# Performance work log

Hardware: AMD Instinct MI355X
Metric: run time of the kernel (lower is better)

Reference implementation:

```python
import jax, jax.numpy as jnp
import numpy as np

SPINS = (16, 16)
D_FEAT = 1024
H1 = (4096, 4096, 2048)
H2 = (2048, 1)


def _pair_idx(n):
    # Matches: idx_h1 = [i for i in range(n-1) for j in range(n-1-i)]
    #          h2 = concat(h[k:] for k in 1..n-1)  -> all ordered pairs (i, j), i < j
    i = np.repeat(np.arange(n - 1), np.arange(n - 1, 0, -1))
    j = np.concatenate([np.arange(k + 1, n) for k in range(n - 1)])
    return i.astype(np.int32), j.astype(np.int32)


def setup_inputs():
    key = jax.random.key(0)
    ks = jax.random.split(key, 6)

    def w(k, fi, fo, scale):
        return (scale / np.sqrt(fi)).astype(np.float32) * jax.random.normal(k, (fi, fo), jnp.float32)

    d_in = 2 * D_FEAT
    return {
        "h_one": jax.random.normal(ks[0], (sum(SPINS), D_FEAT), jnp.float32),
        "w1_0": w(ks[1], d_in, H1[0], np.float32(np.sqrt(2.0))),
        "b1_0": jnp.zeros((H1[0],), jnp.float32),
        "w1_1": w(ks[2], H1[0], H1[1], np.float32(np.sqrt(2.0))),
        "b1_1": jnp.zeros((H1[1],), jnp.float32),
        # final mlp1 layer scaled so |hidden| ~ 2: keeps the pair-product finite in fp32
        "w1_2": w(ks[3], H1[1], H1[2], np.float32(2.0)),
        "b1_2": jnp.zeros((H1[2],), jnp.float32),
        "w2_0": w(ks[4], H1[2], H2[0], np.float32(1.0)),
        "b2_0": jnp.zeros((H2[0],), jnp.float32),
        "w2_1": w(ks[5], H2[0], H2[1], np.float32(1.0)),
        "b2_1": jnp.zeros((H2[1],), jnp.float32),
    }


def reference(h_one, w1_0, b1_0, w1_1, b1_1, w1_2, b1_2, w2_0, b2_0, w2_1, b2_1):
    def mlp1(x):  # silu hidden layers, linear output
        x = jax.nn.silu(x @ w1_0 + b1_0)
        x = jax.nn.silu(x @ w1_1 + b1_1)
        return x @ w1_2 + b1_2

    def mlp2(x):  # tanh hidden layer, linear scalar output
        x = jnp.tanh(x @ w2_0 + b2_0)
        return x @ w2_1 + b2_1

    sumlogA = jnp.float32(0.0)
    off = 0
    for n in SPINS:  # fixed, small, structurally distinct loop over spin channels
        h = h_one[off:off + n]
        off += n
        ii, jj = _pair_idx(n)  # static numpy indices
        h1, h2 = h[ii], h[jj]  # [P, D] pairwise gathers, P = n*(n-1)/2
        hidden = mlp1(jnp.concatenate([h1, h2], axis=-1)) \
               - mlp1(jnp.concatenate([h2, h1], axis=-1))  # antisymmetric in (h1, h2)
        a = jnp.prod(hidden, axis=0)  # product-reduce over pairs -> [H1[-1]]
        A = mlp2(a)                   # [1]
        sumlogA = sumlogA + jnp.log(jnp.abs(A)).squeeze()
    return sumlogA
```

## Files before the change

### kernel.cpp

```cpp
#include <hip/hip_runtime.h>
#include <hip/hip_bf16.h>
#include <math.h>


typedef __attribute__((ext_vector_type(8))) short short8;
typedef __attribute__((ext_vector_type(4))) float floatx4;

#define AS1 __attribute__((address_space(1)))
#define AS3 __attribute__((address_space(3)))
#define GLD16(g, l) __builtin_amdgcn_global_load_lds((AS1 const unsigned int*)(g), (AS3 unsigned int*)(l), 16, 0, 0)

__device__ __forceinline__ float silu_f(float x) {
    return x / (1.0f + __expf(-x));
}

__device__ __forceinline__ void split2(float x, unsigned short& hi, unsigned short& lo) {
    unsigned u = __float_as_uint(x);
    unsigned r = u + 0x7FFFu + ((u >> 16) & 1u);
    unsigned short h = (unsigned short)(r >> 16);
    float hf = __uint_as_float((unsigned)h << 16);
    float rem = x - hf;
    unsigned u2 = __float_as_uint(rem);
    unsigned r2 = u2 + 0x7FFFu + ((u2 >> 16) & 1u);
    hi = h;
    lo = (unsigned short)(r2 >> 16);
}

__global__ __launch_bounds__(256)
void transpose_split_all(const float* __restrict__ w10, const float* __restrict__ w11,
                         const float* __restrict__ w12, const float* __restrict__ h_one,
                         unsigned short* __restrict__ t10h, unsigned short* __restrict__ t10l,
                         unsigned short* __restrict__ t11h, unsigned short* __restrict__ t11l,
                         unsigned short* __restrict__ t12h, unsigned short* __restrict__ t12l,
                         unsigned short* __restrict__ Ah, unsigned short* __restrict__ Al) {
    const int t = threadIdx.x;
    int id = blockIdx.x;

    if (id >= 8192) {
        const int base = (id - 8192) * 4096 + t * 16;
        #pragma unroll
        for (int j = 0; j < 4; ++j) {
            const int f = base + 4 * j;
            const int r = f >> 10;
            const int c = f & 1023;
            floatx4 v = __builtin_nontemporal_load((const floatx4*)&h_one[f]);
            ushort4 hv, lv;
            split2(v.x, hv.x, lv.x);
            split2(v.y, hv.y, lv.y);
            split2(v.z, hv.z, lv.z);
            split2(v.w, hv.w, lv.w);
            const size_t o1 = (size_t)r * 2048 + c;
            const size_t o2 = (size_t)(64 + r) * 2048 + 1024 + c;
            *(ushort4*)&Ah[o1] = hv;
            *(ushort4*)&Al[o1] = lv;
            *(ushort4*)&Ah[o2] = hv;
            *(ushort4*)&Al[o2] = lv;
        }
        return;
    }

    const float* W;
    unsigned short *Th, *Tl;
    int K, N, nt, kt;
    if (id < 2048)       { W = w10; Th = t10h; Tl = t10l; K = 2048; N = 4096; nt = id & 63; kt = id >> 6; }
    else if (id < 6144)  { id -= 2048; W = w11; Th = t11h; Tl = t11l; K = 4096; N = 4096; nt = id & 63; kt = id >> 6; }
    else                 { id -= 6144; W = w12; Th = t12h; Tl = t12l; K = 4096; N = 2048; nt = id & 31; kt = id >> 5; }

    __shared__ float tile[64][65];
    const int n0 = nt * 64;
    const int k0 = kt * 64;

    const int lrow = t >> 4;
    const int lcol = (t & 15) * 4;
    #pragma unroll
    for (int p = 0; p < 4; ++p) {
        const int r = p * 16 + lrow;
        floatx4 v = __builtin_nontemporal_load((const floatx4*)&W[(size_t)(k0 + r) * N + n0 + lcol]);
        tile[r][lcol + 0] = v.x;
        tile[r][lcol + 1] = v.y;
        tile[r][lcol + 2] = v.z;
        tile[r][lcol + 3] = v.w;
    }
    __syncthreads();

    const int srow0 = t >> 3;
    const int koff  = (t & 7) * 8;
    #pragma unroll
    for (int p = 0; p < 2; ++p) {
        const int sn = p * 32 + srow0;
        unsigned short hv[8], lv[8];
        #pragma unroll
        for (int kk = 0; kk < 8; ++kk)
            split2(tile[koff + kk][sn], hv[kk], lv[kk]);
        unsigned short* dh = &Th[(size_t)(n0 + sn) * K + k0 + koff];
        unsigned short* dl = &Tl[(size_t)(n0 + sn) * K + k0 + koff];
        *(short8*)dh = *(short8*)&hv[0];
        *(short8*)dl = *(short8*)&lv[0];
    }
}

__global__ __launch_bounds__(256, 2)
void gemm128(const unsigned short* __restrict__ Ah, const unsigned short* __restrict__ Al,
             const unsigned short* __restrict__ Bh, const unsigned short* __restrict__ Bl,
             int K, float* __restrict__ Cpart, int N, int Mtot, int kc)
{
    __shared__ __align__(16) unsigned short As[2][128][32];
    __shared__ __align__(16) unsigned short Bs[2][128][32];

    const int tid  = threadIdx.x;
    const int lane = tid & 63;
    const int wid  = tid >> 6;
    const int n0 = blockIdx.x * 128;
    const int m0 = blockIdx.y * 128;
    const int kbase = blockIdx.z * kc;

    const int srow   = wid * 32 + (lane >> 2);
    const int schunk = (lane & 3) ^ ((srow >> 1) & 3);
    const unsigned short* gA0h = Ah + (size_t)(m0 + srow) * K + kbase + schunk * 8;
    const unsigned short* gA1h = gA0h + (size_t)16 * K;
    const unsigned short* gA0l = Al + (size_t)(m0 + srow) * K + kbase + schunk * 8;
    const unsigned short* gA1l = gA0l + (size_t)16 * K;
    const unsigned short* gB0h = Bh + (size_t)(n0 + srow) * K + kbase + schunk * 8;
    const unsigned short* gB1h = gB0h + (size_t)16 * K;
    const unsigned short* gB0l = Bl + (size_t)(n0 + srow) * K + kbase + schunk * 8;
    const unsigned short* gB1l = gB0l + (size_t)16 * K;
    unsigned short* lA0h = &As[0][wid * 32][0];
    unsigned short* lA1h = &As[0][wid * 32 + 16][0];
    unsigned short* lA0l = &As[1][wid * 32][0];
    unsigned short* lA1l = &As[1][wid * 32 + 16][0];
    unsigned short* lB0h = &Bs[0][wid * 32][0];
    unsigned short* lB1h = &Bs[0][wid * 32 + 16][0];
    unsigned short* lB0l = &Bs[1][wid * 32][0];
    unsigned short* lB1l = &Bs[1][wid * 32 + 16][0];

    const int mhalf = wid >> 1;
    const int nhalf = wid & 1;
    const int lm = lane & 15;
    const int q  = lane >> 4;
    int aoffs[4], boffs[4];
    #pragma unroll
    for (int f = 0; f < 4; ++f) {
        int arow = mhalf * 64 + f * 16 + lm;
        int aslot = q ^ ((arow >> 1) & 3);
        aoffs[f] = arow * 32 + aslot * 8;
        int brow = nhalf * 64 + f * 16 + lm;
        int bslot = q ^ ((brow >> 1) & 3);
        boffs[f] = brow * 32 + bslot * 8;
    }
    const unsigned short* AsF = &As[0][0][0];
    const unsigned short* BsF = &Bs[0][0][0];

    floatx4 acc[4][4];
    #pragma unroll
    for (int ms = 0; ms < 4; ++ms)
        #pragma unroll
        for (int ns = 0; ns < 4; ++ns)
            acc[ms][ns] = (floatx4){0.f, 0.f, 0.f, 0.f};

    const int S = kc >> 5;
    for (int s = 0; s < S; ++s) {
        const int ko = s << 5;
        __syncthreads();
        GLD16(gA0h + ko, lA0h);
        GLD16(gA1h + ko, lA1h);
        GLD16(gA0l + ko, lA0l);
        GLD16(gA1l + ko, lA1l);
        GLD16(gB0h + ko, lB0h);
        GLD16(gB1h + ko, lB1h);
        GLD16(gB0l + ko, lB0l);
        GLD16(gB1l + ko, lB1l);
        __syncthreads();

        short8 afh[4], afl[4], bfh[4], bfl[4];
        #pragma unroll
        for (int f = 0; f < 4; ++f) {
            afh[f] = *(const short8*)(AsF + aoffs[f]);
            afl[f] = *(const short8*)(AsF + 4096 + aoffs[f]);
            bfh[f] = *(const short8*)(BsF + boffs[f]);
            bfl[f] = *(const short8*)(BsF + 4096 + boffs[f]);
        }
        #pragma unroll
        for (int ms = 0; ms < 4; ++ms)
            #pragma unroll
            for (int ns = 0; ns < 4; ++ns)
                acc[ms][ns] = __builtin_amdgcn_mfma_f32_16x16x32_bf16(afh[ms], bfh[ns], acc[ms][ns], 0, 0, 0);
        #pragma unroll
        for (int ms = 0; ms < 4; ++ms)
            #pragma unroll
            for (int ns = 0; ns < 4; ++ns)
                acc[ms][ns] = __builtin_amdgcn_mfma_f32_16x16x32_bf16(afl[ms], bfh[ns], acc[ms][ns], 0, 0, 0);
        #pragma unroll
        for (int ms = 0; ms < 4; ++ms)
            #pragma unroll
            for (int ns = 0; ns < 4; ++ns)
                acc[ms][ns] = __builtin_amdgcn_mfma_f32_16x16x32_bf16(afh[ms], bfl[ns], acc[ms][ns], 0, 0, 0);
    }

    float* Cp = Cpart + (size_t)blockIdx.z * Mtot * N;
    const int lr = (lane >> 4) * 4;
    #pragma unroll
    for (int ms = 0; ms < 4; ++ms)
        #pragma unroll
        for (int ns = 0; ns < 4; ++ns)
            #pragma unroll
            for (int r = 0; r < 4; ++r)
                Cp[(size_t)(m0 + mhalf * 64 + ms * 16 + lr + r) * N + n0 + nhalf * 64 + ns * 16 + lm] = acc[ms][ns][r];
}

__global__ __launch_bounds__(256)
void build_y1_kernel(const float* __restrict__ PQ, const float* __restrict__ b1,
                     unsigned short* __restrict__ Y1h, unsigned short* __restrict__ Y1l) {
    const int r = blockIdx.x;
    const int g = r / 240;
    const int rem = r % 240;
    const int o = rem / 120;
    const int p = rem % 120;
    int i = 0, pp = p, cnt = 15;
    while (pp >= cnt) { pp -= cnt; cnt--; i++; }
    const int j = i + 1 + pp;
    const int ai = g * 16 + (o ? j : i);
    const int bi = g * 16 + (o ? i : j);
    const size_t chunk4 = (size_t)128 * 4096 / 4;
    const float4* Pr0 = (const float4*)(PQ + (size_t)ai * 4096);
    const float4* Qr0 = (const float4*)(PQ + (size_t)(64 + bi) * 4096);
    const float4* Br  = (const float4*)b1;
    for (int c = threadIdx.x; c < 1024; c += 256) {
        float4 bv = Br[c];
        float s0 = bv.x, s1 = bv.y, s2 = bv.z, s3 = bv.w;
        #pragma unroll
        for (int cc = 0; cc < 4; ++cc) {
            float4 pv = Pr0[c + cc * chunk4];
            float4 qv = Qr0[c + cc * chunk4];
            s0 += pv.x + qv.x;
            s1 += pv.y + qv.y;
            s2 += pv.z + qv.z;
            s3 += pv.w + qv.w;
        }
        s0 = silu_f(s0);
        s1 = silu_f(s1);
        s2 = silu_f(s2);
        s3 = silu_f(s3);
        ushort4 hv, lv;
        split2(s0, hv.x, lv.x);
        split2(s1, hv.y, lv.y);
        split2(s2, hv.z, lv.z);
        split2(s3, hv.w, lv.w);
        *(ushort4*)&Y1h[(size_t)r * 4096 + c * 4] = hv;
        *(ushort4*)&Y1l[(size_t)r * 4096 + c * 4] = lv;
    }
}

__global__ __launch_bounds__(256)
void reduce4_silu_split(const float* __restrict__ Part, const float* __restrict__ bias,
                        unsigned short* __restrict__ Yh, unsigned short* __restrict__ Yl) {
    const size_t idx = (size_t)blockIdx.x * 256 + threadIdx.x;
    const size_t stride4 = (size_t)512 * 4096 / 4;
    const float4* p = (const float4*)Part;
    float4 v0 = p[idx], v1 = p[idx + stride4], v2 = p[idx + 2 * stride4], v3 = p[idx + 3 * stride4];
    const int col = (int)((idx * 4) & 4095);
    float4 b = *(const float4*)&bias[col];
    float s0 = silu_f(v0.x + v1.x + v2.x + v3.x + b.x);
    float s1 = silu_f(v0.y + v1.y + v2.y + v3.y + b.y);
    float s2 = silu_f(v0.z + v1.z + v2.z + v3.z + b.z);
    float s3 = silu_f(v0.w + v1.w + v2.w + v3.w + b.w);
    ushort4 hv, lv;
    split2(s0, hv.x, lv.x);
    split2(s1, hv.y, lv.y);
    split2(s2, hv.z, lv.z);
    split2(s3, hv.w, lv.w);
    *(ushort4*)&Yh[idx * 4] = hv;
    *(ushort4*)&Yl[idx * 4] = lv;
}

__global__ __launch_bounds__(256)
void reduce8_bias(const float* __restrict__ Part, const float* __restrict__ bias,
                  float* __restrict__ Hb) {
    const size_t idx = (size_t)blockIdx.x * 256 + threadIdx.x;
    const size_t stride4 = (size_t)512 * 2048 / 4;
    const float4* p = (const float4*)Part;
    float4 s = p[idx];
    #pragma unroll
    for (int c = 1; c < 8; ++c) {
        float4 v = p[idx + c * stride4];
        s.x += v.x; s.y += v.y; s.z += v.z; s.w += v.w;
    }
    const int col = (int)((idx * 4) & 2047);
    float4 b = *(const float4*)&bias[col];
    s.x += b.x; s.y += b.y; s.z += b.z; s.w += b.w;
    *(float4*)&Hb[idx * 4] = s;
}

__global__ __launch_bounds__(256)
void reduce_prod_kernel(const float* __restrict__ H, float* __restrict__ a_part) {
    const int g = blockIdx.y;
    const int cz = blockIdx.z;
    const int c = blockIdx.x * 256 + threadIdx.x;
    const float* base = H + (size_t)g * 240 * 2048 + c;
    float prod = 1.0f;
    const int p0 = cz * 30;
    for (int p = p0; p < p0 + 30; ++p) {
        float f = base[(size_t)p * 2048] - base[(size_t)(120 + p) * 2048];
        prod *= f;
    }
    a_part[(size_t)((g << 2) | cz) * 2048 + c] = prod;
}

__global__ __launch_bounds__(256)
void mlp2_acc2_kernel(const float* __restrict__ a_part, const float* __restrict__ W,
                      float* __restrict__ Part2) {
    __shared__ float a0s[128], a1s[128];
    const int kc = blockIdx.y, nc = blockIdx.x, t = threadIdx.x;
    if (t < 128) {
        const int k = kc * 128 + t;
        a0s[t] = a_part[k] * a_part[2048 + k] * a_part[4096 + k] * a_part[6144 + k];
        a1s[t] = a_part[8192 + k] * a_part[10240 + k] * a_part[12288 + k] * a_part[14336 + k];
    }
    __syncthreads();
    const int n = nc * 256 + t;
    const float* Wp = W + (size_t)(kc * 128) * 2048 + n;
    float s0 = 0.f, s1 = 0.f;
    #pragma unroll 8
    for (int kk = 0; kk < 128; ++kk) {
        float w = Wp[(size_t)kk * 2048];
        s0 = fmaf(a0s[kk], w, s0);
        s1 = fmaf(a1s[kk], w, s1);
    }
    Part2[kc * 4096 + n] = s0;
    Part2[kc * 4096 + 2048 + n] = s1;
}

__global__ __launch_bounds__(256)
void finalize_kernel(const float* __restrict__ Part2, const float* __restrict__ b2_0,
                     const float* __restrict__ w2_1, const float* __restrict__ b2_1,
                     float* __restrict__ out) {
    __shared__ float red[256];
    const int tid = threadIdx.x;
    float result = 0.0f;
    for (int g = 0; g < 2; ++g) {
        float s = 0.f;
        for (int n = tid; n < 2048; n += 256) {
            float acc = b2_0[n];
            #pragma unroll
            for (int kc = 0; kc < 16; ++kc)
                acc += Part2[kc * 4096 + g * 2048 + n];
            s += tanhf(acc) * w2_1[n];
        }
        red[tid] = s;
        __syncthreads();
        for (int off = 128; off > 0; off >>= 1) {
            if (tid < off) red[tid] += red[tid + off];
            __syncthreads();
        }
        if (tid == 0) result += logf(fabsf(red[0] + b2_1[0]));
        __syncthreads();
    }
    if (tid == 0) out[0] = result;
}

extern "C" void kernel_launch(void* const* d_in, const int* in_sizes, int n_in,
                              void* d_out, int out_size, void* d_ws, size_t ws_size,
                              hipStream_t stream) {
    const float* h_one = (const float*)d_in[0];
    const float* w1_0  = (const float*)d_in[1];
    const float* b1_0  = (const float*)d_in[2];
    const float* w1_1  = (const float*)d_in[3];
    const float* b1_1  = (const float*)d_in[4];
    const float* w1_2  = (const float*)d_in[5];
    const float* b1_2  = (const float*)d_in[6];
    const float* w2_0  = (const float*)d_in[7];
    const float* b2_0  = (const float*)d_in[8];
    const float* w2_1  = (const float*)d_in[9];
    const float* b2_1  = (const float*)d_in[10];
    float* out = (float*)d_out;

    char* ws = (char*)d_ws;
    unsigned short* W10t_h = (unsigned short*)ws;
    unsigned short* W10t_l = W10t_h + (size_t)4096 * 2048;
    float*          PartL1 = (float*)ws;
    ws += (size_t)4096 * 2048 * 2 * 2;
    unsigned short* W11t_h = (unsigned short*)ws;
    unsigned short* W11t_l = W11t_h + (size_t)4096 * 4096;
    float*          PartL2 = (float*)ws;
    ws += (size_t)4096 * 4096 * 2 * 2;
    unsigned short* W12t_h = (unsigned short*)ws;
    unsigned short* W12t_l = W12t_h + (size_t)2048 * 4096;
    ws += (size_t)2048 * 4096 * 2 * 2;
    unsigned short* Ah  = (unsigned short*)ws;  ws += (size_t)128 * 2048 * 2;
    unsigned short* Al  = (unsigned short*)ws;  ws += (size_t)128 * 2048 * 2;
    float* PQ  = (float*)ws;                    ws += (size_t)4 * 128 * 4096 * 4;
    unsigned short* Y1h = (unsigned short*)ws;  ws += (size_t)512 * 4096 * 2;
    unsigned short* Y1l = (unsigned short*)ws;  ws += (size_t)512 * 4096 * 2;
    unsigned short* Y2h = (unsigned short*)ws;  ws += (size_t)512 * 4096 * 2;
    unsigned short* Y2l = (unsigned short*)ws;  ws += (size_t)512 * 4096 * 2;
    float* Hb    = (float*)ws;                  ws += (size_t)512 * 2048 * 4;
    float* a_part = (float*)ws;                 ws += (size_t)8 * 2048 * 4;
    float* Part2 = (float*)ws;                  ws += (size_t)16 * 2 * 2048 * 4;

    hipMemsetAsync(Ah, 0, (size_t)128 * 2048 * 2 * 2, stream);
    transpose_split_all<<<8200, 256, 0, stream>>>(w1_0, w1_1, w1_2, h_one,
                                                  W10t_h, W10t_l, W11t_h, W11t_l,
                                                  W12t_h, W12t_l, Ah, Al);

    gemm128<<<dim3(32, 1, 4), 256, 0, stream>>>(Ah, Al, W10t_h, W10t_l, 2048,
                                                PQ, 4096, 128, 512);
    build_y1_kernel<<<480, 256, 0, stream>>>(PQ, b1_0, Y1h, Y1l);

    gemm128<<<dim3(32, 4, 4), 256, 0, stream>>>(Y1h, Y1l, W11t_h, W11t_l, 4096,
                                                PartL1, 4096, 512, 1024);
    reduce4_silu_split<<<2048, 256, 0, stream>>>(PartL1, b1_1, Y2h, Y2l);

    gemm128<<<dim3(16, 4, 8), 256, 0, stream>>>(Y2h, Y2l, W12t_h, W12t_l, 4096,
                                                PartL2, 2048, 512, 512);
    reduce8_bias<<<1024, 256, 0, stream>>>(PartL2, b1_2, Hb);

    reduce_prod_kernel<<<dim3(8, 2, 4), 256, 0, stream>>>(Hb, a_part);
    mlp2_acc2_kernel<<<dim3(8, 16), 256, 0, stream>>>(a_part, w2_0, Part2);
    finalize_kernel<<<1, 256, 0, stream>>>(Part2, b2_0, w2_1, b2_1, out);
}
```

Before: 332.4 us.

## Fuse split-K reductions into GEMM epilogues via last-block atomic counters

Removes the separate reduce4_silu_split, reduce8_bias and finalize kernels. Each split-K GEMM block now bumps a per-tile atomic counter, and the last block to finish a tile sums all partials, adds the bias, and applies SiLU plus the bf16 split or writes fp32. The mlp2 kernel uses the same last-block pattern to run the final tanh, dot product and log. This saves kernel launches and the extra full passes over partial buffers, at the cost of threadfences, atomics, and a serial tail in the last block of each tile.

```diff
diff --git a/kernel.cpp b/kernel.cpp
--- a/kernel.cpp
+++ b/kernel.cpp
@@ -102,7 +102,10 @@
 __global__ __launch_bounds__(256, 2)
 void gemm128(const unsigned short* __restrict__ Ah, const unsigned short* __restrict__ Al,
              const unsigned short* __restrict__ Bh, const unsigned short* __restrict__ Bl,
-             int K, float* __restrict__ Cpart, int N, int Mtot, int kc)
+             int K, float* __restrict__ Cpart, int N, int Mtot, int kc,
+             int mode, unsigned* __restrict__ cnt, const float* __restrict__ bias,
+             unsigned short* __restrict__ Yh, unsigned short* __restrict__ Yl,
+             float* __restrict__ Fout)
 {
     __shared__ __align__(16) unsigned short As[2][128][32];
     __shared__ __align__(16) unsigned short Bs[2][128][32];
@@ -205,6 +208,48 @@
             #pragma unroll
             for (int r = 0; r < 4; ++r)
                 Cp[(size_t)(m0 + mhalf * 64 + ms * 16 + lr + r) * N + n0 + nhalf * 64 + ns * 16 + lm] = acc[ms][ns][r];
+
+    if (mode == 0) return;
+
+    __threadfence();
+    __syncthreads();
+    __shared__ unsigned winflag;
+    if (tid == 0) {
+        const unsigned tileid = blockIdx.y * gridDim.x + blockIdx.x;
+        winflag = (atomicAdd(&cnt[tileid], 1u) == gridDim.z - 1u) ? 1u : 0u;
+    }
+    __syncthreads();
+    if (!winflag) return;
+    __threadfence();
+
+    const int zparts = (int)gridDim.z;
+    const size_t zs4 = ((size_t)Mtot * N) >> 2;
+    const float4* P4 = (const float4*)Cpart;
+    const float4* B4 = (const float4*)bias;
+    for (int e = tid; e < 128 * 32; e += 256) {
+        const int row = e >> 5;
+        const int c4  = e & 31;
+        const size_t fidx = (((size_t)(m0 + row) * N) >> 2) + (size_t)(n0 >> 2) + c4;
+        float4 s = P4[fidx];
+        for (int z = 1; z < zparts; ++z) {
+            float4 v = P4[fidx + (size_t)z * zs4];
+            s.x += v.x; s.y += v.y; s.z += v.z; s.w += v.w;
+        }
+        float4 b = B4[(n0 >> 2) + c4];
+        s.x += b.x; s.y += b.y; s.z += b.z; s.w += b.w;
+        if (mode == 1) {
+            ushort4 hv, lv;
+            split2(silu_f(s.x), hv.x, lv.x);
+            split2(silu_f(s.y), hv.y, lv.y);
+            split2(silu_f(s.z), hv.z, lv.z);
+            split2(silu_f(s.w), hv.w, lv.w);
+            const size_t o = (size_t)(m0 + row) * N + n0 + c4 * 4;
+            *(ushort4*)&Yh[o] = hv;
+            *(ushort4*)&Yl[o] = lv;
+        } else {
+            *(float4*)&Fout[(size_t)(m0 + row) * N + n0 + c4 * 4] = s;
+        }
+    }
 }
 
 __global__ __launch_bounds__(256)
@@ -251,46 +296,6 @@
 }
 
 __global__ __launch_bounds__(256)
-void reduce4_silu_split(const float* __restrict__ Part, const float* __restrict__ bias,
-                        unsigned short* __restrict__ Yh, unsigned short* __restrict__ Yl) {
-    const size_t idx = (size_t)blockIdx.x * 256 + threadIdx.x;
-    const size_t stride4 = (size_t)512 * 4096 / 4;
-    const float4* p = (const float4*)Part;
-    float4 v0 = p[idx], v1 = p[idx + stride4], v2 = p[idx + 2 * stride4], v3 = p[idx + 3 * stride4];
-    const int col = (int)((idx * 4) & 4095);
-    float4 b = *(const float4*)&bias[col];
-    float s0 = silu_f(v0.x + v1.x + v2.x + v3.x + b.x);
-    float s1 = silu_f(v0.y + v1.y + v2.y + v3.y + b.y);
-    float s2 = silu_f(v0.z + v1.z + v2.z + v3.z + b.z);
-    float s3 = silu_f(v0.w + v1.w + v2.w + v3.w + b.w);
-    ushort4 hv, lv;
-    split2(s0, hv.x, lv.x);
-    split2(s1, hv.y, lv.y);
-    split2(s2, hv.z, lv.z);
-    split2(s3, hv.w, lv.w);
-    *(ushort4*)&Yh[idx * 4] = hv;
-    *(ushort4*)&Yl[idx * 4] = lv;
-}
-
-__global__ __launch_bounds__(256)
-void reduce8_bias(const float* __restrict__ Part, const float* __restrict__ bias,
-                  float* __restrict__ Hb) {
-    const size_t idx = (size_t)blockIdx.x * 256 + threadIdx.x;
-    const size_t stride4 = (size_t)512 * 2048 / 4;
-    const float4* p = (const float4*)Part;
-    float4 s = p[idx];
-    #pragma unroll
-    for (int c = 1; c < 8; ++c) {
-        float4 v = p[idx + c * stride4];
-        s.x += v.x; s.y += v.y; s.z += v.z; s.w += v.w;
-    }
-    const int col = (int)((idx * 4) & 2047);
-    float4 b = *(const float4*)&bias[col];
-    s.x += b.x; s.y += b.y; s.z += b.z; s.w += b.w;
-    *(float4*)&Hb[idx * 4] = s;
-}
-
-__global__ __launch_bounds__(256)
 void reduce_prod_kernel(const float* __restrict__ H, float* __restrict__ a_part) {
     const int g = blockIdx.y;
     const int cz = blockIdx.z;
@@ -307,8 +312,12 @@
 
 __global__ __launch_bounds__(256)
 void mlp2_acc2_kernel(const float* __restrict__ a_part, const float* __restrict__ W,
-                      float* __restrict__ Part2) {
+                      float* __restrict__ Part2, unsigned* __restrict__ cnt,
+                      const float* __restrict__ b2_0, const float* __restrict__ w2_1,
+                      const float* __restrict__ b2_1, float* __restrict__ out) {
     __shared__ float a0s[128], a1s[128];
+    __shared__ float red[256];
+    __shared__ unsigned winflag;
     const int kc = blockIdx.y, nc = blockIdx.x, t = threadIdx.x;
     if (t < 128) {
         const int k = kc * 128 + t;
@@ -327,34 +336,35 @@
     }
     Part2[kc * 4096 + n] = s0;
     Part2[kc * 4096 + 2048 + n] = s1;
-}
-
-__global__ __launch_bounds__(256)
-void finalize_kernel(const float* __restrict__ Part2, const float* __restrict__ b2_0,
-                     const float* __restrict__ w2_1, const float* __restrict__ b2_1,
-                     float* __restrict__ out) {
-    __shared__ float red[256];
-    const int tid = threadIdx.x;
+
+    __threadfence();
+    __syncthreads();
+    if (t == 0)
+        winflag = (atomicAdd(cnt, 1u) == gridDim.x * gridDim.y - 1u) ? 1u : 0u;
+    __syncthreads();
+    if (!winflag) return;
+    __threadfence();
+
     float result = 0.0f;
     for (int g = 0; g < 2; ++g) {
         float s = 0.f;
-        for (int n = tid; n < 2048; n += 256) {
-            float acc = b2_0[n];
+        for (int nn = t; nn < 2048; nn += 256) {
+            float acc = b2_0[nn];
             #pragma unroll
-            for (int kc = 0; kc < 16; ++kc)
-                acc += Part2[kc * 4096 + g * 2048 + n];
-            s += tanhf(acc) * w2_1[n];
-        }
-        red[tid] = s;
+            for (int kcc = 0; kcc < 16; ++kcc)
+                acc += Part2[kcc * 4096 + g * 2048 + nn];
+            s += tanhf(acc) * w2_1[nn];
+        }
+        red[t] = s;
         __syncthreads();
         for (int off = 128; off > 0; off >>= 1) {
-            if (tid < off) red[tid] += red[tid + off];
+            if (t < off) red[t] += red[t + off];
             __syncthreads();
         }
-        if (tid == 0) result += logf(fabsf(red[0] + b2_1[0]));
+        if (t == 0) result += logf(fabsf(red[0] + b2_1[0]));
         __syncthreads();
     }
-    if (tid == 0) out[0] = result;
+    if (t == 0) out[0] = result;
 }
 
 extern "C" void kernel_launch(void* const* d_in, const int* in_sizes, int n_in,
@@ -387,6 +397,10 @@
     ws += (size_t)2048 * 4096 * 2 * 2;
     unsigned short* Ah  = (unsigned short*)ws;  ws += (size_t)128 * 2048 * 2;
     unsigned short* Al  = (unsigned short*)ws;  ws += (size_t)128 * 2048 * 2;
+    unsigned* cntbuf = (unsigned*)ws;           ws += 1024;
+    unsigned* cntL1 = cntbuf;
+    unsigned* cntL2 = cntbuf + 128;
+    unsigned* cntM  = cntbuf + 192;
     float* PQ  = (float*)ws;                    ws += (size_t)4 * 128 * 4096 * 4;
     unsigned short* Y1h = (unsigned short*)ws;  ws += (size_t)512 * 4096 * 2;
     unsigned short* Y1l = (unsigned short*)ws;  ws += (size_t)512 * 4096 * 2;
@@ -396,24 +410,25 @@
     float* a_part = (float*)ws;                 ws += (size_t)8 * 2048 * 4;
     float* Part2 = (float*)ws;                  ws += (size_t)16 * 2 * 2048 * 4;
 
-    hipMemsetAsync(Ah, 0, (size_t)128 * 2048 * 2 * 2, stream);
+    hipMemsetAsync(Ah, 0, (size_t)128 * 2048 * 2 * 2 + 1024, stream);
     transpose_split_all<<<8200, 256, 0, stream>>>(w1_0, w1_1, w1_2, h_one,
                                                   W10t_h, W10t_l, W11t_h, W11t_l,
                                                   W12t_h, W12t_l, Ah, Al);
 
     gemm128<<<dim3(32, 1, 4), 256, 0, stream>>>(Ah, Al, W10t_h, W10t_l, 2048,
-                                                PQ, 4096, 128, 512);
+                                                PQ, 4096, 128, 512,
+                                                0, nullptr, nullptr, nullptr, nullptr, nullptr);
     build_y1_kernel<<<480, 256, 0, stream>>>(PQ, b1_0, Y1h, Y1l);
 
     gemm128<<<dim3(32, 4, 4), 256, 0, stream>>>(Y1h, Y1l, W11t_h, W11t_l, 4096,
-                                                PartL1, 4096, 512, 1024);
-    reduce4_silu_split<<<2048, 256, 0, stream>>>(PartL1, b1_1, Y2h, Y2l);
+                                                PartL1, 4096, 512, 1024,
+                                                1, cntL1, b1_1, Y2h, Y2l, nullptr);
 
     gemm128<<<dim3(16, 4, 8), 256, 0, stream>>>(Y2h, Y2l, W12t_h, W12t_l, 4096,
-                                                PartL2, 2048, 512, 512);
-    reduce8_bias<<<1024, 256, 0, stream>>>(PartL2, b1_2, Hb);
+                                                PartL2, 2048, 512, 512,
+                                                2, cntL2, b1_2, nullptr, nullptr, Hb);
 
     reduce_prod_kernel<<<dim3(8, 2, 4), 256, 0, stream>>>(Hb, a_part);
-    mlp2_acc2_kernel<<<dim3(8, 16), 256, 0, stream>>>(a_part, w2_0, Part2);
-    finalize_kernel<<<1, 256, 0, stream>>>(Part2, b2_0, w2_1, b2_1, out);
-}
+    mlp2_acc2_kernel<<<dim3(8, 16), 256, 0, stream>>>(a_part, w2_0, Part2, cntM,
+                                                      b2_0, w2_1, b2_1, out);
+}
```

Measured after the change: 536.5 us. 1.61x slower.
